# Kernel optimization log

Measured on AMD Instinct MI355X. Metric: run time of the kernel, lower is better.

Reference implementation:

```python
import jax, jax.numpy as jnp
import numpy as np

N0, N1, N2 = 100000, 25000, 5000
E0, E1 = 400000, 80000
IN_FEATS, N_HIDDEN, N_CLASSES = 512, 512, 64


def setup_inputs() -> dict:
    key = jax.random.key(0)
    ks = jax.random.split(key, 16)
    return {
        "feats": jax.random.normal(ks[0], (N0, IN_FEATS), jnp.float32),
        "h0_hist": jax.random.normal(ks[1], (N0, N_HIDDEN), jnp.float32),
        "agg_h0": jax.random.normal(ks[2], (N1, N_HIDDEN), jnp.float32),
        "h1_hist": jax.random.normal(ks[3], (N1, 2 * N_HIDDEN), jnp.float32),
        "agg_h1": jax.random.normal(ks[4], (N2, 2 * N_HIDDEN), jnp.float32),
        "W0": jax.random.normal(ks[5], (N_HIDDEN, IN_FEATS), jnp.float32) * 0.02,
        "b0": jax.random.normal(ks[6], (N_HIDDEN,), jnp.float32) * 0.02,
        "W1": jax.random.normal(ks[7], (N_HIDDEN, N_HIDDEN), jnp.float32) * 0.02,
        "b1": jax.random.normal(ks[8], (N_HIDDEN,), jnp.float32) * 0.02,
        "W2": jax.random.normal(ks[9], (N_CLASSES, 2 * N_HIDDEN), jnp.float32) * 0.02,
        "b2": jax.random.normal(ks[10], (N_CLASSES,), jnp.float32) * 0.02,
        "src0": jax.random.randint(ks[11], (E0,), 0, N0, jnp.int64),
        "dst0": jax.random.randint(ks[12], (E0,), 0, N1, jnp.int64),
        "src1": jax.random.randint(ks[13], (E1,), 0, N1, jnp.int64),
        "dst1": jax.random.randint(ks[14], (E1,), 0, N2, jnp.int64),
    }


def _segment_mean(h_src, src, dst, num_dst):
    # copy_src gather + variable-degree mean reduction (DGL fn.mean)
    msg = h_src[src]  # [E, D]
    sums = jax.ops.segment_sum(msg, dst, num_segments=num_dst)
    deg = jax.ops.segment_sum(jnp.ones((src.shape[0],), h_src.dtype), dst,
                              num_segments=num_dst)
    return sums / jnp.maximum(deg, 1.0)[:, None]


def reference(feats, h0_hist, agg_h0, h1_hist, agg_h1,
              W0, b0, W1, b1, W2, b2,
              src0, dst0, src1, dst1):
    # input layer: linear + relu (dropout=0)
    h = jax.nn.relu(feats @ W0.T + b0)  # [N0, H]

    # block 0: control-variate subtract, mean-aggregate, NodeUpdate(1) concat
    h = h - h0_hist
    agg = _segment_mean(h, src0, dst0, agg_h0.shape[0])  # [N1, H]
    h = (agg + agg_h0) @ W1.T + b1
    h = jnp.concatenate([h, jax.nn.relu(h)], axis=1)  # [N1, 2H]

    # block 1: control-variate subtract, mean-aggregate, NodeUpdate(2)
    h = h - h1_hist
    agg = _segment_mean(h, src1, dst1, agg_h1.shape[0])  # [N2, 2H]
    h = (agg + agg_h1) @ W2.T + b2  # [N2, C]
    return h
```

## Files before the change

### kernel.cpp

```cpp
#include <hip/hip_runtime.h>

#define N0c 100000
#define N1c 25000
#define N2c 5000
#define E0c 400000
#define E1c 80000

typedef __attribute__((ext_vector_type(8))) short bf16x8;
typedef __attribute__((ext_vector_type(4))) float f32x4;

#define GLOAD_LDS(g, l) \
    __builtin_amdgcn_global_load_lds((__attribute__((address_space(1))) const unsigned int*)(const void*)(g), \
                                     (__attribute__((address_space(3))) unsigned int*)(void*)(l), 16, 0, 0)

static __device__ __forceinline__ uint rnd_bf(float f) {
    uint u = __float_as_uint(f);
    return (u + 0x7FFFu + ((u >> 16) & 1u)) & 0xFFFF0000u;
}
static __device__ __forceinline__ unsigned short to_bf(float f) {
    return (unsigned short)(rnd_bf(f) >> 16);
}
static __device__ __forceinline__ uint pk_bf(float f0, float f1) {
    return (rnd_bf(f0) >> 16) | rnd_bf(f1);
}

__global__ __launch_bounds__(256)
void presplit_bf(const float* __restrict__ X, uint4* __restrict__ out,
                 int M, int tile0, int ntiles)
{
    const int id = blockIdx.x * 256 + threadIdx.x;
    const int slot = id & 1023;
    const int tk = id >> 10;
    if (tk >= ntiles * 8) return;
    const int kt8 = tk & 7, mtl = tk >> 3;
    const int r = slot >> 3, p = slot & 7;
    const int o = p ^ (r & 7);
    const int row = (tile0 + mtl) * 128 + r;
    uint4 v = {0u, 0u, 0u, 0u};
    if (row < M) {
        const float* src = X + (size_t)row * 512 + kt8 * 64 + o * 8;
        float4 x0 = *(const float4*)src;
        float4 x1 = *(const float4*)(src + 4);
        v.x = pk_bf(x0.x, x0.y); v.y = pk_bf(x0.z, x0.w);
        v.z = pk_bf(x1.x, x1.y); v.w = pk_bf(x1.z, x1.w);
    }
    out[(size_t)tk * 1024 + slot] = v;
}

template<int SRC, int EPI>
__global__ __launch_bounds__(512, 2)
void gemm_half(const float* __restrict__ Af32, const uint4* __restrict__ At,
               const uint4* __restrict__ Bt, const float* __restrict__ bias,
               const float* __restrict__ hist, unsigned short* __restrict__ C,
               int Mreal, int nblk)
{
    __shared__ uint4 lds[3072];

    const int tid = threadIdx.x;
    const int orig = blockIdx.x;
    const int xcd = orig & 7, q = nblk >> 3, rr = nblk & 7;
    const int lid = (xcd < rr ? xcd * (q + 1) : rr * (q + 1) + (xcd - rr) * q) + (orig >> 3);
    const int bm = lid >> 1, bnh = lid & 1;

    const int w = tid >> 6, lane = tid & 63;
    const int wm = w >> 2, wn = w & 3;
    const int lg = lane >> 4, lr = lane & 15;
    const int sw = lr & 15 & 7;

    const int ar = tid >> 3;
    const int as = tid & 7;

    f32x4 acc[4][4];
#pragma unroll
    for (int i = 0; i < 4; ++i)
#pragma unroll
        for (int j = 0; j < 4; ++j) acc[i][j] = {0.f, 0.f, 0.f, 0.f};

    for (int kt = 0; kt < 8; ++kt) {
        if (kt) __syncthreads();
        if (SRC == 0) {
#pragma unroll
            for (int u = 0; u < 2; ++u) {
                const int r = ar + u * 64;
                const int o = as ^ (r & 7);
                int g = bm * 128 + r; if (g > Mreal - 1) g = Mreal - 1;
                const float* p = Af32 + (size_t)g * 512 + kt * 64 + o * 8;
                float4 x0 = *(const float4*)p;
                float4 x1 = *(const float4*)(p + 4);
                uint4 v;
                v.x = pk_bf(x0.x, x0.y); v.y = pk_bf(x0.z, x0.w);
                v.z = pk_bf(x1.x, x1.y); v.w = pk_bf(x1.z, x1.w);
                lds[r * 8 + as] = v;
            }
        } else {
            const uint4* Ablk = At + ((size_t)bm * 8 + kt) * 1024;
            GLOAD_LDS(Ablk + tid, &lds[tid]);
            GLOAD_LDS(Ablk + 512 + tid, &lds[512 + tid]);
        }
#pragma unroll
        for (int j = 0; j < 4; ++j) {
            const int sl = w * 256 + j * 64 + lane;
            const int sub = sl >> 10;
            const int off = sl & 1023;
            GLOAD_LDS(Bt + ((size_t)(2 * bnh + sub) * 8 + kt) * 1024 + off,
                      &lds[1024 + sl]);
        }
        __syncthreads();

        bf16x8 a[4][2], b[4][2];
#pragma unroll
        for (int mi = 0; mi < 4; ++mi) {
            const uint4* rp = &lds[(wm * 64 + mi * 16 + lr) * 8];
            a[mi][0] = *(const bf16x8*)&rp[lg ^ sw];
            a[mi][1] = *(const bf16x8*)&rp[(4 + lg) ^ sw];
        }
#pragma unroll
        for (int ni = 0; ni < 4; ++ni) {
            const uint4* rp = &lds[1024 + (wn * 64 + ni * 16 + lr) * 8];
            b[ni][0] = *(const bf16x8*)&rp[lg ^ sw];
            b[ni][1] = *(const bf16x8*)&rp[(4 + lg) ^ sw];
        }
#pragma unroll
        for (int kk = 0; kk < 2; ++kk)
#pragma unroll
            for (int mi = 0; mi < 4; ++mi)
#pragma unroll
                for (int ni = 0; ni < 4; ++ni)
                    acc[mi][ni] = __builtin_amdgcn_mfma_f32_16x16x32_bf16(
                        a[mi][kk], b[ni][kk], acc[mi][ni], 0, 0, 0);
    }

#pragma unroll
    for (int mi = 0; mi < 4; ++mi)
#pragma unroll
        for (int ni = 0; ni < 4; ++ni) {
            const int col = bnh * 256 + wn * 64 + ni * 16 + lr;
            const float bv = bias[col];
#pragma unroll
            for (int r = 0; r < 4; ++r) {
                const int m = bm * 128 + wm * 64 + mi * 16 + lg * 4 + r;
                if (m < Mreal) {
                    const float v = acc[mi][ni][r] + bv;
                    if (EPI == 0) {
                        C[(size_t)m * 512 + col] = to_bf(fmaxf(v, 0.f) - hist[(size_t)m * 512 + col]);
                    } else {
                        C[(size_t)m * 1024 + col]       = to_bf(v - hist[(size_t)m * 1024 + col]);
                        C[(size_t)m * 1024 + 512 + col] = to_bf(fmaxf(v, 0.f) - hist[(size_t)m * 1024 + 512 + col]);
                    }
                }
            }
        }
}

__global__ __launch_bounds__(256)
void gemm64(const float* __restrict__ A, const float* __restrict__ B,
            const float* __restrict__ bias, float* __restrict__ C, int M)
{
    const int K = 1024;
    __shared__ float As[32][68];
    __shared__ float Bs[32][68];
    const int tid = threadIdx.x;
    const int tx = tid & 15, ty = tid >> 4;
    const int lrow = tid >> 3;
    const int lk   = (tid & 7) * 4;
    const int bm = blockIdx.x;

    float acc[4][4];
#pragma unroll
    for (int i = 0; i < 4; ++i)
#pragma unroll
        for (int j = 0; j < 4; ++j) acc[i][j] = 0.f;

    int ar0 = bm * 64 + lrow;      if (ar0 > M - 1) ar0 = M - 1;
    int ar1 = bm * 64 + 32 + lrow; if (ar1 > M - 1) ar1 = M - 1;

    for (int kt = 0; kt < K; kt += 32) {
        float4 a0 = *(const float4*)(A + (size_t)ar0 * K + kt + lk);
        float4 a1 = *(const float4*)(A + (size_t)ar1 * K + kt + lk);
        float4 b0 = *(const float4*)(B + (size_t)lrow * K + kt + lk);
        float4 b1 = *(const float4*)(B + (size_t)(32 + lrow) * K + kt + lk);
        __syncthreads();
        As[lk+0][lrow]    = a0.x; As[lk+1][lrow]    = a0.y; As[lk+2][lrow]    = a0.z; As[lk+3][lrow]    = a0.w;
        As[lk+0][lrow+32] = a1.x; As[lk+1][lrow+32] = a1.y; As[lk+2][lrow+32] = a1.z; As[lk+3][lrow+32] = a1.w;
        Bs[lk+0][lrow]    = b0.x; Bs[lk+1][lrow]    = b0.y; Bs[lk+2][lrow]    = b0.z; Bs[lk+3][lrow]    = b0.w;
        Bs[lk+0][lrow+32] = b1.x; Bs[lk+1][lrow+32] = b1.y; Bs[lk+2][lrow+32] = b1.z; Bs[lk+3][lrow+32] = b1.w;
        __syncthreads();
#pragma unroll
        for (int kk = 0; kk < 32; ++kk) {
            float4 av = *(const float4*)&As[kk][ty * 4];
            float4 bv = *(const float4*)&Bs[kk][tx * 4];
            float aa[4] = {av.x, av.y, av.z, av.w};
            float bb[4] = {bv.x, bv.y, bv.z, bv.w};
#pragma unroll
            for (int i = 0; i < 4; ++i)
#pragma unroll
                for (int j = 0; j < 4; ++j)
                    acc[i][j] += aa[i] * bb[j];
        }
    }

    const float4 bv = *(const float4*)&bias[tx * 4];
#pragma unroll
    for (int i = 0; i < 4; ++i) {
        const int m = bm * 64 + ty * 4 + i;
        if (m >= M) continue;
        float4 o;
        o.x = acc[i][0] + bv.x; o.y = acc[i][1] + bv.y;
        o.z = acc[i][2] + bv.z; o.w = acc[i][3] + bv.w;
        *(float4*)&C[(size_t)m * 64 + tx * 4] = o;
    }
}

__global__ void count_deg(const int* __restrict__ dst, int* __restrict__ deg, int E)
{
    int e = blockIdx.x * blockDim.x + threadIdx.x;
    if (e < E) atomicAdd(&deg[dst[e]], 1);
}

__global__ __launch_bounds__(1024)
void exscan(const int* __restrict__ deg, int* __restrict__ off, int* __restrict__ cur, int n)
{
    __shared__ int wsum[16];
    __shared__ int carry;
    const int tid = threadIdx.x, lane = tid & 63, w = tid >> 6;
    if (tid == 0) carry = 0;
    __syncthreads();
    for (int base = 0; base < n; base += 1024) {
        const int i = base + tid;
        const int v = (i < n) ? deg[i] : 0;
        int x = v;
#pragma unroll
        for (int d = 1; d < 64; d <<= 1) {
            int y = __shfl_up(x, d, 64);
            if (lane >= d) x += y;
        }
        if (lane == 63) wsum[w] = x;
        __syncthreads();
        int wo = 0, tot = 0;
#pragma unroll
        for (int k = 0; k < 16; ++k) { int s = wsum[k]; tot += s; if (k < w) wo += s; }
        const int excl = carry + wo + x - v;
        if (i < n) { off[i] = excl; cur[i] = excl; }
        __syncthreads();
        if (tid == 0) carry += tot;
        __syncthreads();
    }
    if (tid == 0) off[n] = carry;
}

__global__ void scatter_edges(const int* __restrict__ src, const int* __restrict__ dst,
                              int* __restrict__ cur, int* __restrict__ eidx, int E)
{
    int e = blockIdx.x * blockDim.x + threadIdx.x;
    if (e < E) {
        int p = atomicAdd(&cur[dst[e]], 1);
        eidx[p] = src[e];
    }
}

__global__ __launch_bounds__(256)
void seg_mean_split(const unsigned short* __restrict__ h, const int* __restrict__ off,
                    const int* __restrict__ eidx, const float* __restrict__ addin,
                    uint4* __restrict__ out, int n_dst, int n_pad)
{
    const int wid = blockIdx.x * 4 + (threadIdx.x >> 6);
    const int lane = threadIdx.x & 63;
    if (wid >= n_pad) return;
    uint4 v = {0u, 0u, 0u, 0u};
    if (wid < n_dst) {
        const int e0 = off[wid], e1 = off[wid + 1];
        float s[8];
#pragma unroll
        for (int i = 0; i < 8; ++i) s[i] = 0.f;
        for (int e = e0; e < e1; ++e) {
            const uint4 vv = *((const uint4*)(h + (size_t)eidx[e] * 512) + lane);
            const uint u[4] = {vv.x, vv.y, vv.z, vv.w};
#pragma unroll
            for (int i = 0; i < 4; ++i) {
                s[2 * i]     += __uint_as_float(u[i] << 16);
                s[2 * i + 1] += __uint_as_float(u[i] & 0xFFFF0000u);
            }
        }
        const float sc = 1.0f / (float)((e1 - e0) > 0 ? (e1 - e0) : 1);
        const float* ad = addin + (size_t)wid * 512 + lane * 8;
        float4 d0 = *(const float4*)ad;
        float4 d1 = *(const float4*)(ad + 4);
        v.x = pk_bf(s[0] * sc + d0.x, s[1] * sc + d0.y);
        v.y = pk_bf(s[2] * sc + d0.z, s[3] * sc + d0.w);
        v.z = pk_bf(s[4] * sc + d1.x, s[5] * sc + d1.y);
        v.w = pk_bf(s[6] * sc + d1.z, s[7] * sc + d1.w);
    }
    const int mt = wid >> 7, r = wid & 127;
    const int kt8 = lane >> 3, o = lane & 7;
    out[((size_t)(mt * 8 + kt8)) * 1024 + r * 8 + (o ^ (r & 7))] = v;
}

__global__ __launch_bounds__(256)
void seg_mean_add4(const unsigned short* __restrict__ h, const int* __restrict__ off,
                   const int* __restrict__ eidx, const float* __restrict__ addin,
                   float* __restrict__ out, int n_dst)
{
    const int wid = blockIdx.x * 4 + (threadIdx.x >> 6);
    const int lane = threadIdx.x & 63;
    if (wid >= n_dst) return;
    const int e0 = off[wid], e1 = off[wid + 1];
    float s[16];
#pragma unroll
    for (int i = 0; i < 16; ++i) s[i] = 0.f;
    for (int e = e0; e < e1; ++e) {
        const uint4* row = (const uint4*)(h + (size_t)eidx[e] * 1024);
#pragma unroll
        for (int half = 0; half < 2; ++half) {
            const uint4 v = row[lane + 64 * half];
            const uint u[4] = {v.x, v.y, v.z, v.w};
#pragma unroll
            for (int i = 0; i < 4; ++i) {
                s[8 * half + 2 * i]     += __uint_as_float(u[i] << 16);
                s[8 * half + 2 * i + 1] += __uint_as_float(u[i] & 0xFFFF0000u);
            }
        }
    }
    const float sc = 1.0f / (float)((e1 - e0) > 0 ? (e1 - e0) : 1);
#pragma unroll
    for (int half = 0; half < 2; ++half) {
        const float* ad = addin + (size_t)wid * 1024 + half * 512 + lane * 8;
        float* o = out + (size_t)wid * 1024 + half * 512 + lane * 8;
        float4 d0 = *(const float4*)ad;
        float4 d1 = *(const float4*)(ad + 4);
        float4 r0, r1;
        r0.x = s[8*half+0] * sc + d0.x; r0.y = s[8*half+1] * sc + d0.y;
        r0.z = s[8*half+2] * sc + d0.z; r0.w = s[8*half+3] * sc + d0.w;
        r1.x = s[8*half+4] * sc + d1.x; r1.y = s[8*half+5] * sc + d1.y;
        r1.z = s[8*half+6] * sc + d1.z; r1.w = s[8*half+7] * sc + d1.w;
        *(float4*)o = r0;
        *(float4*)(o + 4) = r1;
    }
}

extern "C" void kernel_launch(void* const* d_in, const int* in_sizes, int n_in,
                              void* d_out, int out_size, void* d_ws, size_t ws_size,
                              hipStream_t stream)
{
    const float* feats   = (const float*)d_in[0];
    const float* h0_hist = (const float*)d_in[1];
    const float* agg_h0  = (const float*)d_in[2];
    const float* h1_hist = (const float*)d_in[3];
    const float* agg_h1  = (const float*)d_in[4];
    const float* W0 = (const float*)d_in[5];
    const float* b0 = (const float*)d_in[6];
    const float* W1 = (const float*)d_in[7];
    const float* b1 = (const float*)d_in[8];
    const float* W2 = (const float*)d_in[9];
    const float* b2 = (const float*)d_in[10];
    const int* src0 = (const int*)d_in[11];
    const int* dst0 = (const int*)d_in[12];
    const int* src1 = (const int*)d_in[13];
    const int* dst1 = (const int*)d_in[14];

    const int MT1 = 782;
    const int MT2 = 196;
    const size_t TILEB = 8 * 1024 * 16;

    const size_t h0B   = ((size_t)N0c * 512 * 2 + 255) & ~(size_t)255;
    const size_t a2B   = (size_t)MT2 * TILEB;
    const size_t agg1B = (size_t)N2c * 1024 * 4;
    const size_t wsB   = 4 * 8 * 1024 * 16;

    char* ws = (char*)d_ws;
    unsigned short* h0 = (unsigned short*)ws;
    unsigned short* h1cat = h0;                              ws += h0B;
    uint4* A2s    = (uint4*)ws;                              ws += a2B;
    float* agg1   = (float*)ws;                              ws += agg1B;
    uint4* Ws0    = (uint4*)ws;                              ws += wsB;
    uint4* Ws1    = (uint4*)ws;                              ws += wsB;
    int* deg0  = (int*)ws;  ws += sizeof(int) * N1c;
    int* off0  = (int*)ws;  ws += sizeof(int) * (N1c + 1);
    int* cur0  = (int*)ws;  ws += sizeof(int) * N1c;
    int* eidx0 = (int*)ws;  ws += sizeof(int) * E0c;
    int* deg1  = (int*)ws;  ws += sizeof(int) * N2c;
    int* off1  = (int*)ws;  ws += sizeof(int) * (N2c + 1);
    int* cur1  = (int*)ws;  ws += sizeof(int) * N2c;
    int* eidx1 = (int*)ws;

    hipMemsetAsync(deg0, 0, sizeof(int) * N1c, stream);
    hipMemsetAsync(deg1, 0, sizeof(int) * N2c, stream);

    presplit_bf<<<4 * 32, 256, 0, stream>>>(W0, Ws0, 512, 0, 4);
    presplit_bf<<<4 * 32, 256, 0, stream>>>(W1, Ws1, 512, 0, 4);
    count_deg<<<(E0c + 255) / 256, 256, 0, stream>>>(dst0, deg0, E0c);
    exscan<<<1, 1024, 0, stream>>>(deg0, off0, cur0, N1c);
    scatter_edges<<<(E0c + 255) / 256, 256, 0, stream>>>(src0, dst0, cur0, eidx0, E0c);

    gemm_half<0, 0><<<MT1 * 2, 512, 0, stream>>>(feats, nullptr, Ws0, b0, h0_hist, h0, N0c, MT1 * 2);

    seg_mean_split<<<(MT2 * 128) / 4, 256, 0, stream>>>(h0, off0, eidx0, agg_h0, A2s, N1c, MT2 * 128);

    count_deg<<<(E1c + 255) / 256, 256, 0, stream>>>(dst1, deg1, E1c);
    exscan<<<1, 1024, 0, stream>>>(deg1, off1, cur1, N2c);
    scatter_edges<<<(E1c + 255) / 256, 256, 0, stream>>>(src1, dst1, cur1, eidx1, E1c);

    gemm_half<1, 1><<<MT2 * 2, 512, 0, stream>>>(nullptr, A2s, Ws1, b1, h1_hist, h1cat, N1c, MT2 * 2);

    seg_mean_add4<<<(N2c + 3) / 4, 256, 0, stream>>>(h1cat, off1, eidx1, agg_h1, agg1, N2c);

    gemm64<<<(N2c + 63) / 64, 256, 0, stream>>>(agg1, W2, b2, (float*)d_out, N2c);
}
```

Baseline: 639.0 us.

## Fuse GEMM column halves into full-width 1024-thread tiles with direct fp32 LDS staging

Each GEMM block now covers all 512 output columns with 16 waves instead of splitting N across two blocks. The A operand is therefore read from global memory once rather than twice. For the first layer, fp32 features are copied straight into LDS with async global-to-LDS loads and converted to bf16 after the LDS read, replacing the register conversion and store. The K step is halved to 32, which needs a new tile layout for the presplit weights and the aggregated activations, and bf16 packing now uses the hardware v_cvt_pk_bf16_f32 instruction. In exchange there are twice as many barriers and 1024-thread blocks, which may limit occupancy and latency hiding.

After: 1.437 ms. 2.25x slower.

```diff
diff --git a/kernel.cpp b/kernel.cpp
--- a/kernel.cpp
+++ b/kernel.cpp
@@ -20,55 +20,49 @@
 static __device__ __forceinline__ unsigned short to_bf(float f) {
     return (unsigned short)(rnd_bf(f) >> 16);
 }
-static __device__ __forceinline__ uint pk_bf(float f0, float f1) {
-    return (rnd_bf(f0) >> 16) | rnd_bf(f1);
+static __device__ __forceinline__ uint cvt2bf(float f0, float f1) {
+    uint r;
+    asm("v_cvt_pk_bf16_f32 %0, %1, %2" : "=v"(r) : "v"(f0), "v"(f1));
+    return r;
 }
 
 __global__ __launch_bounds__(256)
-void presplit_bf(const float* __restrict__ X, uint4* __restrict__ out,
-                 int M, int tile0, int ntiles)
+void presplit_w(const float* __restrict__ X, uint4* __restrict__ out)
 {
     const int id = blockIdx.x * 256 + threadIdx.x;
-    const int slot = id & 1023;
-    const int tk = id >> 10;
-    if (tk >= ntiles * 8) return;
-    const int kt8 = tk & 7, mtl = tk >> 3;
-    const int r = slot >> 3, p = slot & 7;
-    const int o = p ^ (r & 7);
-    const int row = (tile0 + mtl) * 128 + r;
-    uint4 v = {0u, 0u, 0u, 0u};
-    if (row < M) {
-        const float* src = X + (size_t)row * 512 + kt8 * 64 + o * 8;
-        float4 x0 = *(const float4*)src;
-        float4 x1 = *(const float4*)(src + 4);
-        v.x = pk_bf(x0.x, x0.y); v.y = pk_bf(x0.z, x0.w);
-        v.z = pk_bf(x1.x, x1.y); v.w = pk_bf(x1.z, x1.w);
-    }
-    out[(size_t)tk * 1024 + slot] = v;
-}
-
-template<int SRC, int EPI>
-__global__ __launch_bounds__(512, 2)
-void gemm_half(const float* __restrict__ Af32, const uint4* __restrict__ At,
-               const uint4* __restrict__ Bt, const float* __restrict__ bias,
-               const float* __restrict__ hist, unsigned short* __restrict__ C,
-               int Mreal, int nblk)
-{
-    __shared__ uint4 lds[3072];
+    const int kt = id >> 11;
+    const int sl = id & 2047;
+    const int o = sl >> 9, R = sl & 511;
+    const float* src = X + (size_t)R * 512 + kt * 32 + o * 8;
+    float4 x0 = *(const float4*)src;
+    float4 x1 = *(const float4*)(src + 4);
+    uint4 v;
+    v.x = cvt2bf(x0.x, x0.y); v.y = cvt2bf(x0.z, x0.w);
+    v.z = cvt2bf(x1.x, x1.y); v.w = cvt2bf(x1.z, x1.w);
+    out[id] = v;
+}
+
+template<int ASRC, int EPI>
+__global__ __launch_bounds__(1024, 8)
+void gemm_fused(const float* __restrict__ Af32, const uint4* __restrict__ At,
+                const uint4* __restrict__ Bt, const float* __restrict__ bias,
+                const float* __restrict__ hist, unsigned short* __restrict__ C,
+                int Mreal, int nblk)
+{
+    constexpr int ABASE = (ASRC == 0) ? 1024 : 512;
+    __shared__ uint4 lds[(ASRC == 0) ? 3072 : 2560];
 
     const int tid = threadIdx.x;
     const int orig = blockIdx.x;
     const int xcd = orig & 7, q = nblk >> 3, rr = nblk & 7;
-    const int lid = (xcd < rr ? xcd * (q + 1) : rr * (q + 1) + (xcd - rr) * q) + (orig >> 3);
-    const int bm = lid >> 1, bnh = lid & 1;
+    const int bm = (xcd < rr ? xcd * (q + 1) : rr * (q + 1) + (xcd - rr) * q) + (orig >> 3);
 
     const int w = tid >> 6, lane = tid & 63;
-    const int wm = w >> 2, wn = w & 3;
+    const int wm = w >> 3, wn = w & 7;
     const int lg = lane >> 4, lr = lane & 15;
-    const int sw = lr & 15 & 7;
-
-    const int ar = tid >> 3;
-    const int as = tid & 7;
+
+    const int s_o = tid >> 7, s_r = tid & 127;
+    int s_g = bm * 128 + s_r; if (s_g > Mreal - 1) s_g = Mreal - 1;
 
     f32x4 acc[4][4];
 #pragma unroll
@@ -76,65 +70,54 @@
 #pragma unroll
         for (int j = 0; j < 4; ++j) acc[i][j] = {0.f, 0.f, 0.f, 0.f};
 
-    for (int kt = 0; kt < 8; ++kt) {
+    for (int kt = 0; kt < 16; ++kt) {
         if (kt) __syncthreads();
-        if (SRC == 0) {
-#pragma unroll
-            for (int u = 0; u < 2; ++u) {
-                const int r = ar + u * 64;
-                const int o = as ^ (r & 7);
-                int g = bm * 128 + r; if (g > Mreal - 1) g = Mreal - 1;
-                const float* p = Af32 + (size_t)g * 512 + kt * 64 + o * 8;
-                float4 x0 = *(const float4*)p;
-                float4 x1 = *(const float4*)(p + 4);
+        if (ASRC == 0) {
+            GLOAD_LDS(Af32 + (size_t)s_g * 512 + kt * 32 + s_o * 4, &lds[tid]);
+        } else {
+            if (tid < 512)
+                GLOAD_LDS(At + ((size_t)bm * 16 + kt) * 512 + tid, &lds[tid]);
+        }
+        {
+            const uint4* Bsrc = Bt + (size_t)kt * 2048;
+            GLOAD_LDS(Bsrc + tid, &lds[ABASE + tid]);
+            GLOAD_LDS(Bsrc + 1024 + tid, &lds[ABASE + 1024 + tid]);
+        }
+        __syncthreads();
+
+        bf16x8 a[4], b[4];
+#pragma unroll
+        for (int mi = 0; mi < 4; ++mi) {
+            const int R = wm * 64 + mi * 16 + lr;
+            if (ASRC == 0) {
+                const f32x4 q0 = *(const f32x4*)&lds[(2 * lg) * 128 + R];
+                const f32x4 q1 = *(const f32x4*)&lds[(2 * lg + 1) * 128 + R];
                 uint4 v;
-                v.x = pk_bf(x0.x, x0.y); v.y = pk_bf(x0.z, x0.w);
-                v.z = pk_bf(x1.x, x1.y); v.w = pk_bf(x1.z, x1.w);
-                lds[r * 8 + as] = v;
+                v.x = cvt2bf(q0[0], q0[1]); v.y = cvt2bf(q0[2], q0[3]);
+                v.z = cvt2bf(q1[0], q1[1]); v.w = cvt2bf(q1[2], q1[3]);
+                a[mi] = *(const bf16x8*)&v;
+            } else {
+                a[mi] = *(const bf16x8*)&lds[lg * 128 + R];
             }
-        } else {
-            const uint4* Ablk = At + ((size_t)bm * 8 + kt) * 1024;
-            GLOAD_LDS(Ablk + tid, &lds[tid]);
-            GLOAD_LDS(Ablk + 512 + tid, &lds[512 + tid]);
-        }
-#pragma unroll
-        for (int j = 0; j < 4; ++j) {
-            const int sl = w * 256 + j * 64 + lane;
-            const int sub = sl >> 10;
-            const int off = sl & 1023;
-            GLOAD_LDS(Bt + ((size_t)(2 * bnh + sub) * 8 + kt) * 1024 + off,
-                      &lds[1024 + sl]);
-        }
-        __syncthreads();
-
-        bf16x8 a[4][2], b[4][2];
-#pragma unroll
-        for (int mi = 0; mi < 4; ++mi) {
-            const uint4* rp = &lds[(wm * 64 + mi * 16 + lr) * 8];
-            a[mi][0] = *(const bf16x8*)&rp[lg ^ sw];
-            a[mi][1] = *(const bf16x8*)&rp[(4 + lg) ^ sw];
         }
 #pragma unroll
         for (int ni = 0; ni < 4; ++ni) {
-            const uint4* rp = &lds[1024 + (wn * 64 + ni * 16 + lr) * 8];
-            b[ni][0] = *(const bf16x8*)&rp[lg ^ sw];
-            b[ni][1] = *(const bf16x8*)&rp[(4 + lg) ^ sw];
-        }
-#pragma unroll
-        for (int kk = 0; kk < 2; ++kk)
-#pragma unroll
-            for (int mi = 0; mi < 4; ++mi)
-#pragma unroll
-                for (int ni = 0; ni < 4; ++ni)
-                    acc[mi][ni] = __builtin_amdgcn_mfma_f32_16x16x32_bf16(
-                        a[mi][kk], b[ni][kk], acc[mi][ni], 0, 0, 0);
+            const int Rb = wn * 64 + ni * 16 + lr;
+            b[ni] = *(const bf16x8*)&lds[ABASE + lg * 512 + Rb];
+        }
+#pragma unroll
+        for (int mi = 0; mi < 4; ++mi)
+#pragma unroll
+            for (int ni = 0; ni < 4; ++ni)
+                acc[mi][ni] = __builtin_amdgcn_mfma_f32_16x16x32_bf16(
+                    a[mi], b[ni], acc[mi][ni], 0, 0, 0);
     }
 
 #pragma unroll
     for (int mi = 0; mi < 4; ++mi)
 #pragma unroll
         for (int ni = 0; ni < 4; ++ni) {
-            const int col = bnh * 256 + wn * 64 + ni * 16 + lr;
+            const int col = wn * 64 + ni * 16 + lr;
             const float bv = bias[col];
 #pragma unroll
             for (int r = 0; r < 4; ++r) {
@@ -285,14 +268,14 @@
         const float* ad = addin + (size_t)wid * 512 + lane * 8;
         float4 d0 = *(const float4*)ad;
         float4 d1 = *(const float4*)(ad + 4);
-        v.x = pk_bf(s[0] * sc + d0.x, s[1] * sc + d0.y);
-        v.y = pk_bf(s[2] * sc + d0.z, s[3] * sc + d0.w);
-        v.z = pk_bf(s[4] * sc + d1.x, s[5] * sc + d1.y);
-        v.w = pk_bf(s[6] * sc + d1.z, s[7] * sc + d1.w);
+        v.x = cvt2bf(s[0] * sc + d0.x, s[1] * sc + d0.y);
+        v.y = cvt2bf(s[2] * sc + d0.z, s[3] * sc + d0.w);
+        v.z = cvt2bf(s[4] * sc + d1.x, s[5] * sc + d1.y);
+        v.w = cvt2bf(s[6] * sc + d1.z, s[7] * sc + d1.w);
     }
     const int mt = wid >> 7, r = wid & 127;
-    const int kt8 = lane >> 3, o = lane & 7;
-    out[((size_t)(mt * 8 + kt8)) * 1024 + r * 8 + (o ^ (r & 7))] = v;
+    const int kt = lane >> 2, o = lane & 3;
+    out[((size_t)mt * 16 + kt) * 512 + o * 128 + r] = v;
 }
 
 __global__ __launch_bounds__(256)
@@ -359,12 +342,11 @@
 
     const int MT1 = 782;
     const int MT2 = 196;
-    const size_t TILEB = 8 * 1024 * 16;
 
     const size_t h0B   = ((size_t)N0c * 512 * 2 + 255) & ~(size_t)255;
-    const size_t a2B   = (size_t)MT2 * TILEB;
+    const size_t a2B   = (size_t)MT2 * 16 * 512 * 16;
     const size_t agg1B = (size_t)N2c * 1024 * 4;
-    const size_t wsB   = 4 * 8 * 1024 * 16;
+    const size_t wsB   = 16 * 2048 * 16;
 
     char* ws = (char*)d_ws;
     unsigned short* h0 = (unsigned short*)ws;
@@ -385,13 +367,13 @@
     hipMemsetAsync(deg0, 0, sizeof(int) * N1c, stream);
     hipMemsetAsync(deg1, 0, sizeof(int) * N2c, stream);
 
-    presplit_bf<<<4 * 32, 256, 0, stream>>>(W0, Ws0, 512, 0, 4);
-    presplit_bf<<<4 * 32, 256, 0, stream>>>(W1, Ws1, 512, 0, 4);
+    presplit_w<<<128, 256, 0, stream>>>(W0, Ws0);
+    presplit_w<<<128, 256, 0, stream>>>(W1, Ws1);
     count_deg<<<(E0c + 255) / 256, 256, 0, stream>>>(dst0, deg0, E0c);
     exscan<<<1, 1024, 0, stream>>>(deg0, off0, cur0, N1c);
     scatter_edges<<<(E0c + 255) / 256, 256, 0, stream>>>(src0, dst0, cur0, eidx0, E0c);
 
-    gemm_half<0, 0><<<MT1 * 2, 512, 0, stream>>>(feats, nullptr, Ws0, b0, h0_hist, h0, N0c, MT1 * 2);
+    gemm_fused<0, 0><<<MT1, 1024, 0, stream>>>(feats, nullptr, Ws0, b0, h0_hist, h0, N0c, MT1);
 
     seg_mean_split<<<(MT2 * 128) / 4, 256, 0, stream>>>(h0, off0, eidx0, agg_h0, A2s, N1c, MT2 * 128);
 
@@ -399,7 +381,7 @@
     exscan<<<1, 1024, 0, stream>>>(deg1, off1, cur1, N2c);
     scatter_edges<<<(E1c + 255) / 256, 256, 0, stream>>>(src1, dst1, cur1, eidx1, E1c);
 
-    gemm_half<1, 1><<<MT2 * 2, 512, 0, stream>>>(nullptr, A2s, Ws1, b1, h1_hist, h1cat, N1c, MT2 * 2);
+    gemm_fused<1, 1><<<MT2, 1024, 0, stream>>>(nullptr, A2s, Ws1, b1, h1_hist, h1cat, N1c, MT2);
 
     seg_mean_add4<<<(N2c + 3) / 4, 256, 0, stream>>>(h1cat, off1, eidx1, agg_h1, agg1, N2c);
 
```
